# Kernel optimization log

Hardware: AMD Instinct MI355X
Metric: run time of the kernel (lower is better)

The kernel has to match this reference:

```python
import jax, jax.numpy as jnp
import numpy as np
import math

MAXL = 3
TAUS = [16, 16, 16, 16]
OUT_TAUS = [16, 16, 16, 16]
BM_CNT = 1.0
BM_EPS = 1e-5

# (l1, l2, l) triples in the kernel's triple-loop order, bucketed by output l
TRIPLES = {l: [] for l in range(MAXL + 1)}
for _l1 in range(MAXL + 1):
    for _l2 in range(_l1 + 1):
        for _l in range(_l1 - _l2, min(_l1 + _l2, MAXL) + 1):
            TRIPLES[_l].append((_l1, _l2))

MIDDLE_TAUS = [sum(TAUS[a] * TAUS[b] for (a, b) in TRIPLES[l]) for l in range(MAXL + 1)]


def _cg_coef(l1, m1, l2, m2, l, m):
    if m1 + m2 != m:
        return 0.0
    f = math.factorial
    pre = math.sqrt((2 * l + 1) * f(l1 + l2 - l) * f(l1 - l2 + l) * f(-l1 + l2 + l) / f(l1 + l2 + l + 1))
    pre *= math.sqrt(f(l + m) * f(l - m) * f(l1 - m1) * f(l1 + m1) * f(l2 - m2) * f(l2 + m2))
    s = 0.0
    for k in range(0, l1 + l2 - l + 1):
        d = [k, l1 + l2 - l - k, l1 - m1 - k, l2 + m2 - k, l - l2 + m1 + k, l - l1 - m2 + k]
        if any(x < 0 for x in d):
            continue
        den = 1.0
        for x in d:
            den *= f(x)
        s += (-1.0) ** k / den
    return pre * s


def _cg_tensor(l1, l2, l):
    t = np.zeros((2 * l1 + 1, 2 * l2 + 1, 2 * l + 1), dtype=np.float32)
    for i, m1 in enumerate(range(-l1, l1 + 1)):
        for j, m2 in enumerate(range(-l2, l2 + 1)):
            m = m1 + m2
            if -l <= m <= l:
                t[i, j, m + l] = _cg_coef(l1, m1, l2, m2, l, m)
    return t

CG = {}
for _l in range(MAXL + 1):
    for (_l1, _l2) in TRIPLES[_l]:
        CG[(_l1, _l2, _l)] = jnp.asarray(_cg_tensor(_l1, _l2, _l))

# complex-multiply contraction tensor: (a*b)[k] = a[i] b[j] CM[i,j,k]
_CM = np.zeros((2, 2, 2), dtype=np.float32)
_CM[0, 0, 0] = 1.0; _CM[1, 1, 0] = -1.0; _CM[0, 1, 1] = 1.0; _CM[1, 0, 1] = 1.0
CM = jnp.asarray(_CM)


def setup_inputs() -> dict:
    key = jax.random.key(0)
    k1, k2, k3 = jax.random.split(key, 3)
    in_len = sum(TAUS[l] * (2 * l + 1) for l in range(MAXL + 1))  # 256
    wlen = sum(OUT_TAUS[l] * MIDDLE_TAUS[l] for l in range(MAXL + 1))  # 90112
    activations = jax.random.normal(k1, (2048, in_len, 2), dtype=jnp.float32)
    W = 0.05 * jax.random.uniform(k2, (wlen, 2), dtype=jnp.float32)
    bn_stds = jax.random.uniform(k3, (sum(MIDDLE_TAUS),), dtype=jnp.float32)
    return {"activations": activations, "W": W, "bn_stds": bn_stds}


def reference(activations, W, bn_stds):
    B = activations.shape[0]
    # split input into per-l parts: [B, tau_l, 2l+1, 2]
    Fs = []
    st = 0
    for l in range(MAXL + 1):
        ln = TAUS[l] * (2 * l + 1)
        Fs.append(activations[:, st:st + ln, :].reshape(B, TAUS[l], 2 * l + 1, 2))
        st += ln
    outs = []
    w_st = 0
    s_st = 0
    for l in range(MAXL + 1):
        # Clebsch-Gordan products feeding output degree l
        mids = []
        for (l1, l2) in TRIPLES[l]:
            c = jnp.einsum('btmi,bsnj,mnp,ijk->btspk', Fs[l1], Fs[l2], CG[(l1, l2, l)], CM)
            mids.append(c.reshape(B, TAUS[l1] * TAUS[l2], 2 * l + 1, 2))
        mid = jnp.concatenate(mids, axis=1)  # [B, M_l, 2l+1, 2]
        Ml = MIDDLE_TAUS[l]
        # fused batchnorm: per-middle-channel std over batch and m, moving average update
        batch_std = jnp.sqrt(jnp.mean(jnp.sum(mid * mid, axis=-1), axis=(0, 2)))  # [M_l]
        mov = bn_stds[s_st:s_st + Ml]
        new_std = (mov * BM_CNT + batch_std) / (BM_CNT + 1.0)
        mid = mid / (new_std + BM_EPS)[None, :, None, None]
        # complex linear mix over middle channels -> out_taus[l]
        wl = jax.lax.dynamic_slice_in_dim(W, w_st, OUT_TAUS[l] * Ml, axis=0).reshape(OUT_TAUS[l], Ml, 2)
        out_l = jnp.einsum('oci,bcmj,ijk->bomk', wl, mid, CM)
        outs.append(out_l.reshape(B, OUT_TAUS[l] * (2 * l + 1), 2))
        w_st += OUT_TAUS[l] * Ml
        s_st += Ml
    return jnp.concatenate(outs, axis=1)  # [B, 256, 2]
```

## Files before the change

kernel.cpp:

```cpp
#include <hip/hip_runtime.h>
#include <math.h>

typedef __attribute__((ext_vector_type(8))) short bf16x8;
typedef __attribute__((ext_vector_type(4))) float f32x4;

constexpr double cfact(int n){ double r=1.0; for(int i=2;i<=n;++i) r*=(double)i; return r; }
constexpr double csqrt_(double x){ double g=(x>1.0)?x:1.0; for(int i=0;i<100;++i) g=0.5*(g+x/g); return g; }
constexpr double cg_coef_(int l1,int m1,int l2,int m2,int l,int m){
  double pre = csqrt_((double)(2*l+1)*cfact(l1+l2-l)*cfact(l1-l2+l)*cfact(-l1+l2+l)/cfact(l1+l2+l+1));
  pre = pre*csqrt_(cfact(l+m)*cfact(l-m)*cfact(l1-m1)*cfact(l1+m1)*cfact(l2-m2)*cfact(l2+m2));
  double s=0.0;
  for(int k=0;k<=l1+l2-l;++k){
    int d0=k,d1=l1+l2-l-k,d2=l1-m1-k,d3=l2+m2-k,d4=l-l2+m1+k,d5=l-l1-m2+k;
    if(d0<0||d1<0||d2<0||d3<0||d4<0||d5<0) continue;
    double den=cfact(d0)*cfact(d1)*cfact(d2)*cfact(d3)*cfact(d4)*cfact(d5);
    s+=((k&1)?-1.0:1.0)/den;
  }
  return pre*s;
}
struct CGList{ int n; float coef[64]; int mi[64]; int ni[64]; int pi[64]; };
constexpr CGList build_cg(int l1,int l2,int l){
  CGList T{};
  for(int i=0;i<2*l1+1;++i){
    for(int j=0;j<2*l2+1;++j){
      int m1=i-l1, m2=j-l2, m=m1+m2;
      if(m<-l||m>l) continue;
      double c=cg_coef_(l1,m1,l2,m2,l,m);
      if(c>1e-12||c<-1e-12){
        T.coef[T.n]=(float)c; T.mi[T.n]=i; T.ni[T.n]=j; T.pi[T.n]=m+l; T.n++;
      }
    }
  }
  return T;
}

__device__ __host__ constexpr int AOFF(int l){ return l==0?0: l==1?16: l==2?64:144; }
__device__ __host__ constexpr int MLs(int l){ return l==0?1024: l==1?1536: l==2?1792:1536; }
__device__ __host__ constexpr int WOFF(int l){ return l==0?0: l==1?16384: l==2?40960:69632; }
__device__ __host__ constexpr int SOFF(int l){ return l==0?0: l==1?1024: l==2?2560:4352; }
__device__ __host__ constexpr int ABASE(int l){ return l==0?0: l==1?65536: l==2?163840:278528; }

#define DEVFN __device__ __forceinline__
#define BP 68
#define AP 68

DEVFN unsigned f2bf2(float x, float y){
  unsigned ux = __float_as_uint(x); ux = (ux + 0x7FFFu + ((ux>>16)&1u)) >> 16;
  unsigned uy = __float_as_uint(y); uy = (uy + 0x7FFFu + ((uy>>16)&1u)) >> 16;
  return (ux & 0xFFFFu) | (uy << 16);
}

template<int L1,int L2,int L>
DEVFN void cg_accum(const float2* F1, const float2* F2, float2* mid){
  constexpr CGList T = build_cg(L1,L2,L);
  #pragma unroll
  for(int e=0;e<T.n;++e){
    const float c = T.coef[e];
    const float2 a = F1[T.mi[e]];
    const float2 b = F2[T.ni[e]];
    float pr = a.x*b.x - a.y*b.y;
    float pim= a.x*b.y + a.y*b.x;
    mid[T.pi[e]].x += c*pr;
    mid[T.pi[e]].y += c*pim;
  }
}

template<int L1,int L2,int L>
DEVFN void k1_body(const float2* __restrict__ acts, int u, int bh,
                   float& ssa, float& ssb){
  constexpr int N1=2*L1+1, N2=2*L2+1, NP=2*L+1;
  const int t = u>>3, s0 = (u&7)*2;
  #pragma unroll 2
  for(int bi=0;bi<8;++bi){
    const int row = bh*8 + bi;
    const float2* arow = acts + row*256;
    float2 F1[N1], F2a[N2], F2b[N2], mida[NP], midb[NP];
    #pragma unroll
    for(int m=0;m<N1;++m) F1[m]=arow[AOFF(L1)+t*N1+m];
    #pragma unroll
    for(int n=0;n<N2;++n){
      F2a[n]=arow[AOFF(L2)+s0*N2+n];
      F2b[n]=arow[AOFF(L2)+(s0+1)*N2+n];
    }
    #pragma unroll
    for(int p=0;p<NP;++p){ mida[p]=make_float2(0.f,0.f); midb[p]=make_float2(0.f,0.f); }
    cg_accum<L1,L2,L>(F1,F2a,mida);
    cg_accum<L1,L2,L>(F1,F2b,midb);
    #pragma unroll
    for(int p=0;p<NP;++p){
      ssa += mida[p].x*mida[p].x + mida[p].y*mida[p].y;
      ssb += midb[p].x*midb[p].x + midb[p].y*midb[p].y;
    }
  }
}

template<int L1,int L2,int L>
DEVFN void k1_quad(const float* __restrict__ act, float2* acts, int b0,
                   int u, int bh, float& ssa, float& ssb){
  const int tid = threadIdx.x;
  for(int seg=0; seg<4; ++seg){
    const float4* ag = (const float4*)act + (size_t)(b0+seg*16)*128;
    float4* as4 = (float4*)acts;
    #pragma unroll
    for(int j=0;j<8;++j) as4[j*256+tid] = ag[j*256+tid];
    __syncthreads();
    k1_body<L1,L2,L>(acts,u,bh,ssa,ssb);
    __syncthreads();
  }
}

__global__ __launch_bounds__(256) void k_sumsq(const float* __restrict__ act,
                                               float2* __restrict__ part){
  __shared__ float2 acts[16*256];
  int bid=blockIdx.x;
  const int order[23] = {22,16,21,18,15,20,13,9,14,8,17,7,12,6,10,3,5,19,2,11,1,4,0};
  int ti = order[bid>>5];
  int chunk = bid&31;
  int b0 = chunk*64;
  const int tid = threadIdx.x;
  const int u = tid & 127, bh = tid >> 7;
  float ssa=0.f, ssb=0.f;
  switch(ti){
    case 0:  k1_quad<0,0,0>(act,acts,b0,u,bh,ssa,ssb); break;
    case 1:  k1_quad<1,1,0>(act,acts,b0,u,bh,ssa,ssb); break;
    case 2:  k1_quad<2,2,0>(act,acts,b0,u,bh,ssa,ssb); break;
    case 3:  k1_quad<3,3,0>(act,acts,b0,u,bh,ssa,ssb); break;
    case 4:  k1_quad<1,0,1>(act,acts,b0,u,bh,ssa,ssb); break;
    case 5:  k1_quad<1,1,1>(act,acts,b0,u,bh,ssa,ssb); break;
    case 6:  k1_quad<2,1,1>(act,acts,b0,u,bh,ssa,ssb); break;
    case 7:  k1_quad<2,2,1>(act,acts,b0,u,bh,ssa,ssb); break;
    case 8:  k1_quad<3,2,1>(act,acts,b0,u,bh,ssa,ssb); break;
    case 9:  k1_quad<3,3,1>(act,acts,b0,u,bh,ssa,ssb); break;
    case 10: k1_quad<1,1,2>(act,acts,b0,u,bh,ssa,ssb); break;
    case 11: k1_quad<2,0,2>(act,acts,b0,u,bh,ssa,ssb); break;
    case 12: k1_quad<2,1,2>(act,acts,b0,u,bh,ssa,ssb); break;
    case 13: k1_quad<2,2,2>(act,acts,b0,u,bh,ssa,ssb); break;
    case 14: k1_quad<3,1,2>(act,acts,b0,u,bh,ssa,ssb); break;
    case 15: k1_quad<3,2,2>(act,acts,b0,u,bh,ssa,ssb); break;
    case 16: k1_quad<3,3,2>(act,acts,b0,u,bh,ssa,ssb); break;
    case 17: k1_quad<2,1,3>(act,acts,b0,u,bh,ssa,ssb); break;
    case 18: k1_quad<2,2,3>(act,acts,b0,u,bh,ssa,ssb); break;
    case 19: k1_quad<3,0,3>(act,acts,b0,u,bh,ssa,ssb); break;
    case 20: k1_quad<3,1,3>(act,acts,b0,u,bh,ssa,ssb); break;
    case 21: k1_quad<3,2,3>(act,acts,b0,u,bh,ssa,ssb); break;
    default: k1_quad<3,3,3>(act,acts,b0,u,bh,ssa,ssb); break;
  }
  part[(size_t)((ti*32 + chunk)*2 + bh)*128 + u] = make_float2(ssa, ssb);
}

__global__ __launch_bounds__(256) void k_buildA(const float* __restrict__ W,
                                                const float* __restrict__ bn,
                                                const float2* __restrict__ part,
                                                short* __restrict__ A){
  int idx = blockIdx.x*256 + threadIdx.x;
  if(idx>=5888) return;
  int ti = idx>>8, ch = idx&255, u = ch>>1;
  const float2* ps = part + (size_t)(ti*64)*128 + u;
  float sum = 0.f;
  #pragma unroll 8
  for(int j=0;j<64;++j){
    float2 v = ps[(size_t)j*128];
    sum += (ch&1) ? v.y : v.x;
  }
  int l = (idx<1024)?0 : (idx<2560)?1 : (idx<4352)?2 : 3;
  float divi = (l==0)?(1.f/2048.f) : (l==1)?(1.f/6144.f) : (l==2)?(1.f/10240.f) : (1.f/14336.f);
  float bstd = sqrtf(sum*divi);
  float nstd = 0.5f*(bn[idx]+bstd);
  float s = 1.f/(nstd+1e-5f);
  int c = idx - SOFF(l);
  int Ml = MLs(l);
  const float2* wbase = (const float2*)W + WOFF(l) + c;
  unsigned* Aw = (unsigned*)(A + ABASE(l));
  for(int o=0;o<16;++o){
    float2 w = wbase[(size_t)o*Ml];
    Aw[(size_t)o*Ml + c]      = f2bf2(w.x*s, -w.y*s);
    Aw[(size_t)(o+16)*Ml + c] = f2bf2(w.y*s,  w.x*s);
  }
}


#define SA_B   0
#define BT_B   16384
#define LA_B   33792

template<int NTIL>
DEVFN void kf_pre(const float* __restrict__ act, char* smem, int b0){
  const int tid = threadIdx.x;
  const float2* actg2 = (const float2*)act + (size_t)b0*256;
  float4* s4 = (float4*)(smem + SA_B);
  const float4* ag = (const float4*)actg2;
  #pragma unroll
  for(int j=0;j<4;++j) s4[j*256+tid] = ag[j*256+tid];
  unsigned* btile = (unsigned*)(smem + BT_B);
  for(int i=tid; i<NTIL*16*BP; i+=256) btile[i]=0;
  __syncthreads();
}

template<int L1,int L2,int L,int Q,int NTIL>
DEVFN void kf_triple(char* smem, const unsigned* __restrict__ Aw,
                     f32x4& cR, f32x4& cI){
  constexpr int N1=2*L1+1, N2=2*L2+1, NP=2*L+1;
  constexpr int Ml = MLs(L);
  const float2* sa = (const float2*)(smem + SA_B);
  unsigned* btile  = (unsigned*)(smem + BT_B);
  unsigned* ldsA   = (unsigned*)(smem + LA_B);
  const int tid = threadIdx.x;
  const int lane = tid & 63, w = tid >> 6;
  const int col = lane & 15, quad = lane >> 4;
  const int up = tid & 31, bi = tid >> 5;
  const int r0 = tid>>4,       j0 = (tid&15)*4;
  const int r1 = (tid+256)>>4;
  {
    const int base = (Q*4)*64;
    uint4 v0 = *(const uint4*)(Aw + (size_t)r0*Ml + base + j0);
    uint4 v1 = *(const uint4*)(Aw + (size_t)r1*Ml + base + j0);
    *(uint4*)(ldsA + r0*AP + j0) = v0;
    *(uint4*)(ldsA + r1*AP + j0) = v1;
  }
  #pragma unroll 1
  for(int cc=0; cc<4; ++cc){
    unsigned* cbuf = ldsA + (cc&1)*(32*AP);
    unsigned* nbuf = ldsA + ((cc+1)&1)*(32*AP);
    uint4 v0, v1;
    if(cc<3){
      const int base = (Q*4+cc+1)*64;
      v0 = *(const uint4*)(Aw + (size_t)r0*Ml + base + j0);
      v1 = *(const uint4*)(Aw + (size_t)r1*Ml + base + j0);
    }
    {
      const int u = cc*32 + up;
      const int t = u>>3, s0 = (u&7)*2;
      const float2* arow = sa + bi*256;
      float2 F1[N1], F2a[N2], F2b[N2], mida[NP], midb[NP];
      #pragma unroll
      for(int m=0;m<N1;++m) F1[m]=arow[AOFF(L1)+t*N1+m];
      #pragma unroll
      for(int n=0;n<N2;++n){
        F2a[n]=arow[AOFF(L2)+s0*N2+n];
        F2b[n]=arow[AOFF(L2)+(s0+1)*N2+n];
      }
      #pragma unroll
      for(int p=0;p<NP;++p){ mida[p]=make_float2(0.f,0.f); midb[p]=make_float2(0.f,0.f); }
      cg_accum<L1,L2,L>(F1,F2a,mida);
      cg_accum<L1,L2,L>(F1,F2b,midb);
      #pragma unroll
      for(int p=0;p<NP;++p){
        uint2 v; v.x = f2bf2(mida[p].x, mida[p].y); v.y = f2bf2(midb[p].x, midb[p].y);
        *(uint2*)(btile + (size_t)(bi*NP+p)*BP + 2*up) = v;
      }
    }
    if(cc<3){
      *(uint4*)(nbuf + r0*AP + j0) = v0;
      *(uint4*)(nbuf + r1*AP + j0) = v1;
    }
    __syncthreads();
    if(w < NTIL){
      const unsigned* ar0 = cbuf + col*AP + quad*4;
      const unsigned* ar1 = cbuf + (col+16)*AP + quad*4;
      const unsigned* bb  = btile + (w*16+col)*BP + quad*4;
      #pragma unroll
      for(int ks=0; ks<4; ++ks){
        bf16x8 b  = *(const bf16x8*)(bb + ks*16);
        bf16x8 A0 = *(const bf16x8*)(ar0 + ks*16);
        bf16x8 A1 = *(const bf16x8*)(ar1 + ks*16);
        cR = __builtin_amdgcn_mfma_f32_16x16x32_bf16(A0, b, cR, 0, 0, 0);
        cI = __builtin_amdgcn_mfma_f32_16x16x32_bf16(A1, b, cI, 0, 0, 0);
      }
    }
    __syncthreads();
  }
}

template<int L,int NTIL>
DEVFN void kf_epi(float* __restrict__ out, int b0, f32x4 cR, f32x4 cI){
  constexpr int NP = 2*L+1;
  const int tid = threadIdx.x, lane = tid & 63, w = tid >> 6;
  const int col = lane & 15, quad = lane >> 4;
  if(w < NTIL){
    const int r = w*16 + col;
    if(r < 8*NP){
      const int b = b0 + r/NP, p = r - (r/NP)*NP;
      float2* o2 = (float2*)out + (size_t)b*256 + AOFF(L);
      #pragma unroll
      for(int i=0;i<4;++i) o2[(quad*4+i)*NP + p] = make_float2(cR[i], cI[i]);
    }
  }
}

__global__ __launch_bounds__(256,3) void k_fusedall(const float* __restrict__ act,
    const short* __restrict__ A, float* __restrict__ out){
  __shared__ __align__(16) char smem[51200];
  const int bid = blockIdx.x;
  f32x4 cR={0.f,0.f,0.f,0.f}, cI={0.f,0.f,0.f,0.f};
  if(bid < 256){
    const int b0 = bid*8;
    kf_pre<4>(act,smem,b0);
    const unsigned* Aw=(const unsigned*)(A+ABASE(3));
    kf_triple<2,1,3,0,4>(smem,Aw,cR,cI);
    kf_triple<2,2,3,1,4>(smem,Aw,cR,cI);
    kf_triple<3,0,3,2,4>(smem,Aw,cR,cI);
    kf_triple<3,1,3,3,4>(smem,Aw,cR,cI);
    kf_triple<3,2,3,4,4>(smem,Aw,cR,cI);
    kf_triple<3,3,3,5,4>(smem,Aw,cR,cI);
    kf_epi<3,4>(out,b0,cR,cI);
  } else if(bid < 512){
    const int b0 = (bid-256)*8;
    kf_pre<3>(act,smem,b0);
    const unsigned* Aw=(const unsigned*)(A+ABASE(2));
    kf_triple<1,1,2,0,3>(smem,Aw,cR,cI);
    kf_triple<2,0,2,1,3>(smem,Aw,cR,cI);
    kf_triple<2,1,2,2,3>(smem,Aw,cR,cI);
    kf_triple<2,2,2,3,3>(smem,Aw,cR,cI);
    kf_triple<3,1,2,4,3>(smem,Aw,cR,cI);
    kf_triple<3,2,2,5,3>(smem,Aw,cR,cI);
    kf_triple<3,3,2,6,3>(smem,Aw,cR,cI);
    kf_epi<2,3>(out,b0,cR,cI);
  } else if(bid < 768){
    const int b0 = (bid-512)*8;
    kf_pre<2>(act,smem,b0);
    const unsigned* Aw=(const unsigned*)(A+ABASE(1));
    kf_triple<1,0,1,0,2>(smem,Aw,cR,cI);
    kf_triple<1,1,1,1,2>(smem,Aw,cR,cI);
    kf_triple<2,1,1,2,2>(smem,Aw,cR,cI);
    kf_triple<2,2,1,3,2>(smem,Aw,cR,cI);
    kf_triple<3,2,1,4,2>(smem,Aw,cR,cI);
    kf_triple<3,3,1,5,2>(smem,Aw,cR,cI);
    kf_epi<1,2>(out,b0,cR,cI);
  } else {
    const int b0 = (bid-768)*8;
    kf_pre<1>(act,smem,b0);
    const unsigned* Aw=(const unsigned*)(A+ABASE(0));
    kf_triple<0,0,0,0,1>(smem,Aw,cR,cI);
    kf_triple<1,1,0,1,1>(smem,Aw,cR,cI);
    kf_triple<2,2,0,2,1>(smem,Aw,cR,cI);
    kf_triple<3,3,0,3,1>(smem,Aw,cR,cI);
    kf_epi<0,1>(out,b0,cR,cI);
  }
}

extern "C" void kernel_launch(void* const* d_in, const int* in_sizes, int n_in,
                              void* d_out, int out_size, void* d_ws, size_t ws_size,
                              hipStream_t stream) {
  const float* act = (const float*)d_in[0];
  const float* W   = (const float*)d_in[1];
  const float* bn  = (const float*)d_in[2];
  float* out = (float*)d_out;

  short*  A    = (short*)((char*)d_ws + 24576);
  float2* part = (float2*)((char*)d_ws + 1048576);

  hipLaunchKernelGGL(k_sumsq,   dim3(23*32), dim3(256), 0, stream, act, part);
  hipLaunchKernelGGL(k_buildA,  dim3(23),    dim3(256), 0, stream, W, bn, part, A);
  hipLaunchKernelGGL(k_fusedall,dim3(1024),  dim3(256), 0, stream, act, A, out);
}
```

Baseline: 144.7 us.

## Move batchnorm scale into mid tile and overlap weight conversion with sumsq

The sum-of-squares kernel now reads activations directly from global memory instead of staging them through shared memory. It uses twice as many blocks, each covering 32 rows. The weight-to-bf16 conversion moves into extra blocks of that same kernel, so it runs in parallel with the statistics pass. The middle kernel now only computes per-channel scales. The fused GEMM kernel applies these scales to the CG products before bf16 packing, which removes the serial weight rewrite from the critical path. The cost is more global loads in sumsq, an extra multiply per mid element, and slightly different bf16 rounding.

```diff
diff --git a/kernel.cpp b/kernel.cpp
--- a/kernel.cpp
+++ b/kernel.cpp
@@ -66,22 +66,21 @@
 }
 
 template<int L1,int L2,int L>
-DEVFN void k1_body(const float2* __restrict__ acts, int u, int bh,
-                   float& ssa, float& ssb){
+DEVFN void k1g(const float2* __restrict__ act2, int b0, int u, int bh,
+               float& ssa, float& ssb){
   constexpr int N1=2*L1+1, N2=2*L2+1, NP=2*L+1;
   const int t = u>>3, s0 = (u&7)*2;
+  const float2* base1  = act2 + AOFF(L1) + t*N1;
+  const float2* base2a = act2 + AOFF(L2) + s0*N2;
+  const float2* base2b = base2a + N2;
   #pragma unroll 2
-  for(int bi=0;bi<8;++bi){
-    const int row = bh*8 + bi;
-    const float2* arow = acts + row*256;
+  for(int bi=0;bi<16;++bi){
+    const size_t ro = (size_t)(b0 + bh*16 + bi)*256;
     float2 F1[N1], F2a[N2], F2b[N2], mida[NP], midb[NP];
     #pragma unroll
-    for(int m=0;m<N1;++m) F1[m]=arow[AOFF(L1)+t*N1+m];
+    for(int m=0;m<N1;++m) F1[m]=base1[ro+m];
     #pragma unroll
-    for(int n=0;n<N2;++n){
-      F2a[n]=arow[AOFF(L2)+s0*N2+n];
-      F2b[n]=arow[AOFF(L2)+(s0+1)*N2+n];
-    }
+    for(int n=0;n<N2;++n){ F2a[n]=base2a[ro+n]; F2b[n]=base2b[ro+n]; }
     #pragma unroll
     for(int p=0;p<NP;++p){ mida[p]=make_float2(0.f,0.f); midb[p]=make_float2(0.f,0.f); }
     cg_accum<L1,L2,L>(F1,F2a,mida);
@@ -94,88 +93,84 @@
   }
 }
 
-template<int L1,int L2,int L>
-DEVFN void k1_quad(const float* __restrict__ act, float2* acts, int b0,
-                   int u, int bh, float& ssa, float& ssb){
+DEVFN void convW(const float* __restrict__ W, short* __restrict__ A, int idx){
+  int l = (idx<1024)?0 : (idx<2560)?1 : (idx<4352)?2 : 3;
+  int c = idx - SOFF(l);
+  int Ml = MLs(l);
+  const float2* wbase = (const float2*)W + WOFF(l) + c;
+  unsigned* Aw = (unsigned*)(A + ABASE(l));
+  #pragma unroll 4
+  for(int o=0;o<16;++o){
+    float2 w = wbase[(size_t)o*Ml];
+    Aw[(size_t)o*Ml + c]      = f2bf2(w.x, -w.y);
+    Aw[(size_t)(o+16)*Ml + c] = f2bf2(w.y,  w.x);
+  }
+}
+
+__global__ __launch_bounds__(256) void k_sumsq(const float* __restrict__ act,
+                                               float2* __restrict__ part,
+                                               const float* __restrict__ W,
+                                               short* __restrict__ A){
+  const int bid = blockIdx.x;
   const int tid = threadIdx.x;
-  for(int seg=0; seg<4; ++seg){
-    const float4* ag = (const float4*)act + (size_t)(b0+seg*16)*128;
-    float4* as4 = (float4*)acts;
-    #pragma unroll
-    for(int j=0;j<8;++j) as4[j*256+tid] = ag[j*256+tid];
-    __syncthreads();
-    k1_body<L1,L2,L>(acts,u,bh,ssa,ssb);
-    __syncthreads();
-  }
-}
-
-__global__ __launch_bounds__(256) void k_sumsq(const float* __restrict__ act,
-                                               float2* __restrict__ part){
-  __shared__ float2 acts[16*256];
-  int bid=blockIdx.x;
+  if(bid >= 1472){
+    convW(W, A, (bid-1472)*256 + tid);
+    return;
+  }
   const int order[23] = {22,16,21,18,15,20,13,9,14,8,17,7,12,6,10,3,5,19,2,11,1,4,0};
-  int ti = order[bid>>5];
-  int chunk = bid&31;
-  int b0 = chunk*64;
-  const int tid = threadIdx.x;
+  const int ti = order[bid>>6];
+  const int chunk = bid&63;
+  const int b0 = chunk*32;
   const int u = tid & 127, bh = tid >> 7;
+  const float2* act2 = (const float2*)act;
   float ssa=0.f, ssb=0.f;
   switch(ti){
-    case 0:  k1_quad<0,0,0>(act,acts,b0,u,bh,ssa,ssb); break;
-    case 1:  k1_quad<1,1,0>(act,acts,b0,u,bh,ssa,ssb); break;
-    case 2:  k1_quad<2,2,0>(act,acts,b0,u,bh,ssa,ssb); break;
-    case 3:  k1_quad<3,3,0>(act,acts,b0,u,bh,ssa,ssb); break;
-    case 4:  k1_quad<1,0,1>(act,acts,b0,u,bh,ssa,ssb); break;
-    case 5:  k1_quad<1,1,1>(act,acts,b0,u,bh,ssa,ssb); break;
-    case 6:  k1_quad<2,1,1>(act,acts,b0,u,bh,ssa,ssb); break;
-    case 7:  k1_quad<2,2,1>(act,acts,b0,u,bh,ssa,ssb); break;
-    case 8:  k1_quad<3,2,1>(act,acts,b0,u,bh,ssa,ssb); break;
-    case 9:  k1_quad<3,3,1>(act,acts,b0,u,bh,ssa,ssb); break;
-    case 10: k1_quad<1,1,2>(act,acts,b0,u,bh,ssa,ssb); break;
-    case 11: k1_quad<2,0,2>(act,acts,b0,u,bh,ssa,ssb); break;
-    case 12: k1_quad<2,1,2>(act,acts,b0,u,bh,ssa,ssb); break;
-    case 13: k1_quad<2,2,2>(act,acts,b0,u,bh,ssa,ssb); break;
-    case 14: k1_quad<3,1,2>(act,acts,b0,u,bh,ssa,ssb); break;
-    case 15: k1_quad<3,2,2>(act,acts,b0,u,bh,ssa,ssb); break;
-    case 16: k1_quad<3,3,2>(act,acts,b0,u,bh,ssa,ssb); break;
-    case 17: k1_quad<2,1,3>(act,acts,b0,u,bh,ssa,ssb); break;
-    case 18: k1_quad<2,2,3>(act,acts,b0,u,bh,ssa,ssb); break;
-    case 19: k1_quad<3,0,3>(act,acts,b0,u,bh,ssa,ssb); break;
-    case 20: k1_quad<3,1,3>(act,acts,b0,u,bh,ssa,ssb); break;
-    case 21: k1_quad<3,2,3>(act,acts,b0,u,bh,ssa,ssb); break;
-    default: k1_quad<3,3,3>(act,acts,b0,u,bh,ssa,ssb); break;
-  }
-  part[(size_t)((ti*32 + chunk)*2 + bh)*128 + u] = make_float2(ssa, ssb);
-}
-
-__global__ __launch_bounds__(256) void k_buildA(const float* __restrict__ W,
-                                                const float* __restrict__ bn,
-                                                const float2* __restrict__ part,
-                                                short* __restrict__ A){
-  int idx = blockIdx.x*256 + threadIdx.x;
-  if(idx>=5888) return;
-  int ti = idx>>8, ch = idx&255, u = ch>>1;
-  const float2* ps = part + (size_t)(ti*64)*128 + u;
+    case 0:  k1g<0,0,0>(act2,b0,u,bh,ssa,ssb); break;
+    case 1:  k1g<1,1,0>(act2,b0,u,bh,ssa,ssb); break;
+    case 2:  k1g<2,2,0>(act2,b0,u,bh,ssa,ssb); break;
+    case 3:  k1g<3,3,0>(act2,b0,u,bh,ssa,ssb); break;
+    case 4:  k1g<1,0,1>(act2,b0,u,bh,ssa,ssb); break;
+    case 5:  k1g<1,1,1>(act2,b0,u,bh,ssa,ssb); break;
+    case 6:  k1g<2,1,1>(act2,b0,u,bh,ssa,ssb); break;
+    case 7:  k1g<2,2,1>(act2,b0,u,bh,ssa,ssb); break;
+    case 8:  k1g<3,2,1>(act2,b0,u,bh,ssa,ssb); break;
+    case 9:  k1g<3,3,1>(act2,b0,u,bh,ssa,ssb); break;
+    case 10: k1g<1,1,2>(act2,b0,u,bh,ssa,ssb); break;
+    case 11: k1g<2,0,2>(act2,b0,u,bh,ssa,ssb); break;
+    case 12: k1g<2,1,2>(act2,b0,u,bh,ssa,ssb); break;
+    case 13: k1g<2,2,2>(act2,b0,u,bh,ssa,ssb); break;
+    case 14: k1g<3,1,2>(act2,b0,u,bh,ssa,ssb); break;
+    case 15: k1g<3,2,2>(act2,b0,u,bh,ssa,ssb); break;
+    case 16: k1g<3,3,2>(act2,b0,u,bh,ssa,ssb); break;
+    case 17: k1g<2,1,3>(act2,b0,u,bh,ssa,ssb); break;
+    case 18: k1g<2,2,3>(act2,b0,u,bh,ssa,ssb); break;
+    case 19: k1g<3,0,3>(act2,b0,u,bh,ssa,ssb); break;
+    case 20: k1g<3,1,3>(act2,b0,u,bh,ssa,ssb); break;
+    case 21: k1g<3,2,3>(act2,b0,u,bh,ssa,ssb); break;
+    default: k1g<3,3,3>(act2,b0,u,bh,ssa,ssb); break;
+  }
+  part[(size_t)((ti*64 + chunk)*2 + bh)*128 + u] = make_float2(ssa, ssb);
+}
+
+__global__ __launch_bounds__(256) void k_scale(const float* __restrict__ bn,
+                                               const float2* __restrict__ part,
+                                               float* __restrict__ s){
+  const int ti = blockIdx.x;
+  const int ch = threadIdx.x;
+  const int idx = ti*256 + ch;
+  const int u = ch>>1;
+  const float2* ps = part + (size_t)ti*128*128 + u;
   float sum = 0.f;
   #pragma unroll 8
-  for(int j=0;j<64;++j){
-    float2 v = ps[(size_t)j*128];
+  for(int r=0;r<128;++r){
+    float2 v = ps[(size_t)r*128];
     sum += (ch&1) ? v.y : v.x;
   }
   int l = (idx<1024)?0 : (idx<2560)?1 : (idx<4352)?2 : 3;
   float divi = (l==0)?(1.f/2048.f) : (l==1)?(1.f/6144.f) : (l==2)?(1.f/10240.f) : (1.f/14336.f);
   float bstd = sqrtf(sum*divi);
   float nstd = 0.5f*(bn[idx]+bstd);
-  float s = 1.f/(nstd+1e-5f);
-  int c = idx - SOFF(l);
-  int Ml = MLs(l);
-  const float2* wbase = (const float2*)W + WOFF(l) + c;
-  unsigned* Aw = (unsigned*)(A + ABASE(l));
-  for(int o=0;o<16;++o){
-    float2 w = wbase[(size_t)o*Ml];
-    Aw[(size_t)o*Ml + c]      = f2bf2(w.x*s, -w.y*s);
-    Aw[(size_t)(o+16)*Ml + c] = f2bf2(w.y*s,  w.x*s);
-  }
+  s[idx] = 1.f/(nstd+1e-5f);
 }
 
 
@@ -198,7 +193,7 @@
 
 template<int L1,int L2,int L,int Q,int NTIL>
 DEVFN void kf_triple(char* smem, const unsigned* __restrict__ Aw,
-                     f32x4& cR, f32x4& cI){
+                     const float* __restrict__ sg, f32x4& cR, f32x4& cI){
   constexpr int N1=2*L1+1, N2=2*L2+1, NP=2*L+1;
   constexpr int Ml = MLs(L);
   const float2* sa = (const float2*)(smem + SA_B);
@@ -228,6 +223,7 @@
       v1 = *(const uint4*)(Aw + (size_t)r1*Ml + base + j0);
     }
     {
+      const float2 s2 = *(const float2*)(sg + SOFF(L) + Q*256 + cc*64 + 2*up);
       const int u = cc*32 + up;
       const int t = u>>3, s0 = (u&7)*2;
       const float2* arow = sa + bi*256;
@@ -245,7 +241,9 @@
       cg_accum<L1,L2,L>(F1,F2b,midb);
       #pragma unroll
       for(int p=0;p<NP;++p){
-        uint2 v; v.x = f2bf2(mida[p].x, mida[p].y); v.y = f2bf2(midb[p].x, midb[p].y);
+        uint2 v;
+        v.x = f2bf2(mida[p].x*s2.x, mida[p].y*s2.x);
+        v.y = f2bf2(midb[p].x*s2.y, midb[p].y*s2.y);
         *(uint2*)(btile + (size_t)(bi*NP+p)*BP + 2*up) = v;
       }
     }
@@ -288,7 +286,8 @@
 }
 
 __global__ __launch_bounds__(256,3) void k_fusedall(const float* __restrict__ act,
-    const short* __restrict__ A, float* __restrict__ out){
+    const short* __restrict__ A, const float* __restrict__ sg,
+    float* __restrict__ out){
   __shared__ __align__(16) char smem[51200];
   const int bid = blockIdx.x;
   f32x4 cR={0.f,0.f,0.f,0.f}, cI={0.f,0.f,0.f,0.f};
@@ -296,44 +295,44 @@
     const int b0 = bid*8;
     kf_pre<4>(act,smem,b0);
     const unsigned* Aw=(const unsigned*)(A+ABASE(3));
-    kf_triple<2,1,3,0,4>(smem,Aw,cR,cI);
-    kf_triple<2,2,3,1,4>(smem,Aw,cR,cI);
-    kf_triple<3,0,3,2,4>(smem,Aw,cR,cI);
-    kf_triple<3,1,3,3,4>(smem,Aw,cR,cI);
-    kf_triple<3,2,3,4,4>(smem,Aw,cR,cI);
-    kf_triple<3,3,3,5,4>(smem,Aw,cR,cI);
+    kf_triple<2,1,3,0,4>(smem,Aw,sg,cR,cI);
+    kf_triple<2,2,3,1,4>(smem,Aw,sg,cR,cI);
+    kf_triple<3,0,3,2,4>(smem,Aw,sg,cR,cI);
+    kf_triple<3,1,3,3,4>(smem,Aw,sg,cR,cI);
+    kf_triple<3,2,3,4,4>(smem,Aw,sg,cR,cI);
+    kf_triple<3,3,3,5,4>(smem,Aw,sg,cR,cI);
     kf_epi<3,4>(out,b0,cR,cI);
   } else if(bid < 512){
     const int b0 = (bid-256)*8;
     kf_pre<3>(act,smem,b0);
     const unsigned* Aw=(const unsigned*)(A+ABASE(2));
-    kf_triple<1,1,2,0,3>(smem,Aw,cR,cI);
-    kf_triple<2,0,2,1,3>(smem,Aw,cR,cI);
-    kf_triple<2,1,2,2,3>(smem,Aw,cR,cI);
-    kf_triple<2,2,2,3,3>(smem,Aw,cR,cI);
-    kf_triple<3,1,2,4,3>(smem,Aw,cR,cI);
-    kf_triple<3,2,2,5,3>(smem,Aw,cR,cI);
-    kf_triple<3,3,2,6,3>(smem,Aw,cR,cI);
+    kf_triple<1,1,2,0,3>(smem,Aw,sg,cR,cI);
+    kf_triple<2,0,2,1,3>(smem,Aw,sg,cR,cI);
+    kf_triple<2,1,2,2,3>(smem,Aw,sg,cR,cI);
+    kf_triple<2,2,2,3,3>(smem,Aw,sg,cR,cI);
+    kf_triple<3,1,2,4,3>(smem,Aw,sg,cR,cI);
+    kf_triple<3,2,2,5,3>(smem,Aw,sg,cR,cI);
+    kf_triple<3,3,2,6,3>(smem,Aw,sg,cR,cI);
     kf_epi<2,3>(out,b0,cR,cI);
   } else if(bid < 768){
     const int b0 = (bid-512)*8;
     kf_pre<2>(act,smem,b0);
     const unsigned* Aw=(const unsigned*)(A+ABASE(1));
-    kf_triple<1,0,1,0,2>(smem,Aw,cR,cI);
-    kf_triple<1,1,1,1,2>(smem,Aw,cR,cI);
-    kf_triple<2,1,1,2,2>(smem,Aw,cR,cI);
-    kf_triple<2,2,1,3,2>(smem,Aw,cR,cI);
-    kf_triple<3,2,1,4,2>(smem,Aw,cR,cI);
-    kf_triple<3,3,1,5,2>(smem,Aw,cR,cI);
+    kf_triple<1,0,1,0,2>(smem,Aw,sg,cR,cI);
+    kf_triple<1,1,1,1,2>(smem,Aw,sg,cR,cI);
+    kf_triple<2,1,1,2,2>(smem,Aw,sg,cR,cI);
+    kf_triple<2,2,1,3,2>(smem,Aw,sg,cR,cI);
+    kf_triple<3,2,1,4,2>(smem,Aw,sg,cR,cI);
+    kf_triple<3,3,1,5,2>(smem,Aw,sg,cR,cI);
     kf_epi<1,2>(out,b0,cR,cI);
   } else {
     const int b0 = (bid-768)*8;
     kf_pre<1>(act,smem,b0);
     const unsigned* Aw=(const unsigned*)(A+ABASE(0));
-    kf_triple<0,0,0,0,1>(smem,Aw,cR,cI);
-    kf_triple<1,1,0,1,1>(smem,Aw,cR,cI);
-    kf_triple<2,2,0,2,1>(smem,Aw,cR,cI);
-    kf_triple<3,3,0,3,1>(smem,Aw,cR,cI);
+    kf_triple<0,0,0,0,1>(smem,Aw,sg,cR,cI);
+    kf_triple<1,1,0,1,1>(smem,Aw,sg,cR,cI);
+    kf_triple<2,2,0,2,1>(smem,Aw,sg,cR,cI);
+    kf_triple<3,3,0,3,1>(smem,Aw,sg,cR,cI);
     kf_epi<0,1>(out,b0,cR,cI);
   }
 }
@@ -346,10 +345,11 @@
   const float* bn  = (const float*)d_in[2];
   float* out = (float*)d_out;
 
+  float*  s    = (float*)d_ws;
   short*  A    = (short*)((char*)d_ws + 24576);
   float2* part = (float2*)((char*)d_ws + 1048576);
 
-  hipLaunchKernelGGL(k_sumsq,   dim3(23*32), dim3(256), 0, stream, act, part);
-  hipLaunchKernelGGL(k_buildA,  dim3(23),    dim3(256), 0, stream, W, bn, part, A);
-  hipLaunchKernelGGL(k_fusedall,dim3(1024),  dim3(256), 0, stream, act, A, out);
-}
+  hipLaunchKernelGGL(k_sumsq,   dim3(1495), dim3(256), 0, stream, act, part, W, A);
+  hipLaunchKernelGGL(k_scale,   dim3(23),   dim3(256), 0, stream, bn, part, s);
+  hipLaunchKernelGGL(k_fusedall,dim3(1024), dim3(256), 0, stream, act, A, s, out);
+}
```

New measurement: 143.0 us. No clear change (-1.2%).
